# Performance work log

Hardware: AMD Instinct MI355X
Metric: run time of the kernel (lower is better)

## Reference

```python
import jax, jax.numpy as jnp
import numpy as np

NEG_INF = -1.0e12  # matches masked_fill value in the torch module


def _entmax15(x, axis=-1):
    """Exact entmax with alpha=1.5 (Peters & Martins, 2019), sort-based."""
    x = x - jnp.max(x, axis=axis, keepdims=True)
    x = x / 2.0
    d = x.shape[axis]
    xs = -jnp.sort(-x, axis=axis)  # descending sort along normalization axis
    rho = jnp.arange(1, d + 1, dtype=x.dtype)  # 1..d, broadcasts on last axis
    mean = jnp.cumsum(xs, axis=axis) / rho
    mean_sq = jnp.cumsum(xs * xs, axis=axis) / rho
    ss = rho * (mean_sq - mean * mean)
    delta = (1.0 - ss) / rho
    tau = mean - jnp.sqrt(jnp.clip(delta, 0.0))
    support = jnp.sum((tau <= xs).astype(jnp.int32), axis=axis, keepdims=True)
    tau_star = jnp.take_along_axis(tau, support - 1, axis=axis)
    y = jnp.clip(x - tau_star, 0.0)
    return y * y


def setup_inputs() -> dict:
    key = jax.random.key(0)
    kq, kk, kv, km = jax.random.split(key, 4)
    B, H, S, D = 4, 8, 1024, 128
    q = jax.random.normal(kq, (B, H, S, D), dtype=jnp.float32)
    k = jax.random.normal(kk, (B, H, S, D), dtype=jnp.float32)
    v = jax.random.normal(kv, (B, H, S, D), dtype=jnp.float32)
    mask = jax.random.randint(km, (B, 1, S, S), 0, 2, dtype=jnp.int32)
    return {"q": q, "k": k, "v": v, "mask": mask}


def reference(q, k, v, mask):
    D = q.shape[-1]
    scale = 1.0 / jnp.sqrt(jnp.asarray(D, dtype=q.dtype))
    scores = jnp.einsum("bhqd,bhkd->bhqk", q, k) * scale
    scores = jnp.where(mask == 0, jnp.asarray(NEG_INF, dtype=scores.dtype), scores)
    attn = _entmax15(scores, axis=-1)
    return jnp.einsum("bhqk,bhkd->bhqd", attn, v)
```

## Files before the change

### kernel.cpp

```cpp
#include <hip/hip_runtime.h>


#define S_ 1024
#define D_ 128
#define NEG_INF_F (-1.0e12f)
#define SCALE_F 0.08838834764831845f
#define NITER 14

typedef float f32x4 __attribute__((ext_vector_type(4)));
typedef short short8 __attribute__((ext_vector_type(8)));

__device__ __forceinline__ ushort f2bf(float x) {
    unsigned u = __builtin_bit_cast(unsigned, x);
    u += 0x7FFFu + ((u >> 16) & 1u);
    return (ushort)(u >> 16);
}
__device__ __forceinline__ float bf2f(ushort h) {
    unsigned u = ((unsigned)h) << 16;
    return __builtin_bit_cast(float, u);
}

__global__ __launch_bounds__(256)
void pre_cvt(const float* __restrict__ K, const float* __restrict__ V,
             ushort* __restrict__ Kb, ushort* __restrict__ Vt)
{
    __shared__ __align__(16) ushort tileT[64][68];
    const int t = threadIdx.x;
    if (blockIdx.x < 4096) {
        int i = blockIdx.x * 256 + t;
        float4 v = ((const float4*)K)[i];
        ushort4 o;
        o.x = f2bf(v.x); o.y = f2bf(v.y); o.z = f2bf(v.z); o.w = f2bf(v.w);
        ((ushort4*)Kb)[i] = o;
        return;
    }
    const int vb = blockIdx.x - 4096;
    const int bh = vb >> 5, r5 = vb & 31, kt = r5 >> 1, dh = r5 & 1;
    const float* src = V + ((size_t)(bh * S_ + kt * 64)) * D_ + dh * 64;
    #pragma unroll
    for (int i = 0; i < 4; ++i) {
        int idx = t + i * 256, r = idx >> 4, c = idx & 15;
        float4 vv = *(const float4*)(src + (size_t)r * D_ + c * 4);
        tileT[c * 4 + 0][r] = f2bf(vv.x);
        tileT[c * 4 + 1][r] = f2bf(vv.y);
        tileT[c * 4 + 2][r] = f2bf(vv.z);
        tileT[c * 4 + 3][r] = f2bf(vv.w);
    }
    __syncthreads();
    ushort* dst = Vt + ((size_t)(bh * D_ + dh * 64)) * S_ + kt * 64;
    #pragma unroll
    for (int i = 0; i < 2; ++i) {
        int idx = t + i * 256, d = idx >> 3, jj = idx & 7;
        short8 val = *(const short8*)&tileT[d][jj * 8];
        *(short8*)(dst + (size_t)d * S_ + jj * 8) = val;
    }
}

__global__ __launch_bounds__(512, 8)
void entmax_attn(const float* __restrict__ Q, const ushort* __restrict__ Kb,
                 const ushort* __restrict__ Vt, const int* __restrict__ M,
                 float* __restrict__ O)
{
    __shared__ __align__(16) ushort sc[16][1024];
    __shared__ __align__(16) ushort q_s[16][128];

    const int t = threadIdx.x;
    const int w = t >> 6, lane = t & 63, l = lane & 15, quad = lane >> 4;
    const int bh = blockIdx.x >> 6, qt = blockIdx.x & 63, b = bh >> 3;

    const ushort* kb_bh = Kb + (size_t)bh * (S_ * D_);
    const ushort* vt_bh = Vt + (size_t)bh * (D_ * S_);

    {
        const float4* qsrc = (const float4*)(Q + ((size_t)bh * S_ + (size_t)qt * 16) * D_);
        int r = t >> 5, c = t & 31;
        float4 v = qsrc[r * 32 + c];
        ushort4 o;
        o.x = f2bf(v.x); o.y = f2bf(v.y); o.z = f2bf(v.z); o.w = f2bf(v.w);
        *(ushort4*)&q_s[r][(((c >> 1) ^ (r & 7)) << 3) + ((c & 1) << 2)] = o;
    }

    const ushort* kp = kb_bh + (size_t)(w * 16 + l) * D_ + quad * 8;
    short8 c0 = *(const short8*)(kp +  0);
    short8 c1 = *(const short8*)(kp + 32);
    short8 c2 = *(const short8*)(kp + 64);
    short8 c3 = *(const short8*)(kp + 96);

    __syncthreads();

    short8 aq[4];
    #pragma unroll
    for (int ks = 0; ks < 4; ++ks)
        aq[ks] = *(const short8*)&q_s[l][((ks * 4 + quad) ^ (l & 7)) << 3];

    #pragma unroll 1
    for (int kt = 0; kt < 7; ++kt) {
        const ushort* np = kp + (size_t)(kt + 1) * (128 * D_);
        short8 n0 = *(const short8*)(np +  0);
        short8 n1 = *(const short8*)(np + 32);
        short8 n2 = *(const short8*)(np + 64);
        short8 n3 = *(const short8*)(np + 96);
        f32x4 acc = {0.f, 0.f, 0.f, 0.f};
        __builtin_amdgcn_s_setprio(1);
        acc = __builtin_amdgcn_mfma_f32_16x16x32_bf16(aq[0], c0, acc, 0, 0, 0);
        acc = __builtin_amdgcn_mfma_f32_16x16x32_bf16(aq[1], c1, acc, 0, 0, 0);
        acc = __builtin_amdgcn_mfma_f32_16x16x32_bf16(aq[2], c2, acc, 0, 0, 0);
        acc = __builtin_amdgcn_mfma_f32_16x16x32_bf16(aq[3], c3, acc, 0, 0, 0);
        __builtin_amdgcn_s_setprio(0);
        const int coln = kt * 16 + w * 2 + (l >> 3);
        #pragma unroll
        for (int r = 0; r < 4; ++r) {
            const int rr = quad * 4 + r;
            sc[rr][((coln ^ (rr & 7)) << 3) + (l & 7)] = f2bf(acc[r] * SCALE_F);
        }
        c0 = n0; c1 = n1; c2 = n2; c3 = n3;
    }
    {
        f32x4 acc = {0.f, 0.f, 0.f, 0.f};
        __builtin_amdgcn_s_setprio(1);
        acc = __builtin_amdgcn_mfma_f32_16x16x32_bf16(aq[0], c0, acc, 0, 0, 0);
        acc = __builtin_amdgcn_mfma_f32_16x16x32_bf16(aq[1], c1, acc, 0, 0, 0);
        acc = __builtin_amdgcn_mfma_f32_16x16x32_bf16(aq[2], c2, acc, 0, 0, 0);
        acc = __builtin_amdgcn_mfma_f32_16x16x32_bf16(aq[3], c3, acc, 0, 0, 0);
        __builtin_amdgcn_s_setprio(0);
        const int coln = 7 * 16 + w * 2 + (l >> 3);
        #pragma unroll
        for (int r = 0; r < 4; ++r) {
            const int rr = quad * 4 + r;
            sc[rr][((coln ^ (rr & 7)) << 3) + (l & 7)] = f2bf(acc[r] * SCALE_F);
        }
    }
    __syncthreads();

    const int row = t >> 5, u = t & 31;
    const int qg = qt * 16 + row;
    float x[32];
    #pragma unroll
    for (int c = 0; c < 4; ++c) {
        short8 v8 = *(const short8*)&sc[row][((c * 32 + u) ^ (row & 7)) << 3];
        #pragma unroll
        for (int e = 0; e < 8; ++e) x[c * 8 + e] = bf2f(((ushort*)&v8)[e]);
    }
    {
        const int4* mrow = (const int4*)(M + ((size_t)b * S_ + qg) * S_);
        #pragma unroll
        for (int c = 0; c < 4; ++c) {
            #pragma unroll
            for (int h = 0; h < 2; ++h) {
                int4 mm = mrow[c * 64 + u * 2 + h];
                if (mm.x == 0) x[c * 8 + h * 4 + 0] = NEG_INF_F;
                if (mm.y == 0) x[c * 8 + h * 4 + 1] = NEG_INF_F;
                if (mm.z == 0) x[c * 8 + h * 4 + 2] = NEG_INF_F;
                if (mm.w == 0) x[c * 8 + h * 4 + 3] = NEG_INF_F;
            }
        }
    }
    float mx = -3.0e38f;
    #pragma unroll
    for (int j = 0; j < 32; ++j) mx = fmaxf(mx, x[j]);
    #pragma unroll
    for (int off = 1; off < 32; off <<= 1) mx = fmaxf(mx, __shfl_xor(mx, off));
    #pragma unroll
    for (int j = 0; j < 32; ++j) x[j] = (x[j] - mx) * 0.5f;

    float lo = -1.f, hi = 0.f;
    #pragma unroll 1
    for (int it = 0; it < NITER; ++it) {
        const float tm = 0.5f * (lo + hi);
        float f = 0.f;
        #pragma unroll
        for (int j = 0; j < 32; ++j) {
            float d = fmaxf(x[j] - tm, 0.f);
            f = fmaf(d, d, f);
        }
        #pragma unroll
        for (int off = 1; off < 32; off <<= 1) f += __shfl_xor(f, off);
        const bool ge = (f >= 1.f);
        lo = ge ? tm : lo;
        hi = ge ? hi : tm;
    }
    const float tau = 0.5f * (lo + hi);

    #pragma unroll
    for (int c = 0; c < 4; ++c) {
        short8 v8;
        #pragma unroll
        for (int e = 0; e < 8; ++e) {
            float d = fmaxf(x[c * 8 + e] - tau, 0.f);
            ((ushort*)&v8)[e] = f2bf(d * d);
        }
        *(short8*)&sc[row][((c * 32 + u) ^ (row & 7)) << 3] = v8;
    }

    const ushort* vp = vt_bh + (size_t)(w * 16 + l) * S_ + quad * 8;
    c0 = *(const short8*)(vp +  0);
    c1 = *(const short8*)(vp + 32);
    c2 = *(const short8*)(vp + 64);
    c3 = *(const short8*)(vp + 96);
    __syncthreads();

    f32x4 oa = {0.f, 0.f, 0.f, 0.f};
    #pragma unroll 1
    for (int vt = 0; vt < 7; ++vt) {
        const ushort* np = vp + (size_t)(vt + 1) * 128;
        short8 n0 = *(const short8*)(np +  0);
        short8 n1 = *(const short8*)(np + 32);
        short8 n2 = *(const short8*)(np + 64);
        short8 n3 = *(const short8*)(np + 96);
        short8 a0 = *(const short8*)&sc[l][((vt * 16 +  0 + quad) ^ (l & 7)) << 3];
        short8 a1 = *(const short8*)&sc[l][((vt * 16 +  4 + quad) ^ (l & 7)) << 3];
        short8 a2 = *(const short8*)&sc[l][((vt * 16 +  8 + quad) ^ (l & 7)) << 3];
        short8 a3 = *(const short8*)&sc[l][((vt * 16 + 12 + quad) ^ (l & 7)) << 3];
        __builtin_amdgcn_s_setprio(1);
        oa = __builtin_amdgcn_mfma_f32_16x16x32_bf16(a0, c0, oa, 0, 0, 0);
        oa = __builtin_amdgcn_mfma_f32_16x16x32_bf16(a1, c1, oa, 0, 0, 0);
        oa = __builtin_amdgcn_mfma_f32_16x16x32_bf16(a2, c2, oa, 0, 0, 0);
        oa = __builtin_amdgcn_mfma_f32_16x16x32_bf16(a3, c3, oa, 0, 0, 0);
        __builtin_amdgcn_s_setprio(0);
        c0 = n0; c1 = n1; c2 = n2; c3 = n3;
    }
    {
        short8 a0 = *(const short8*)&sc[l][((7 * 16 +  0 + quad) ^ (l & 7)) << 3];
        short8 a1 = *(const short8*)&sc[l][((7 * 16 +  4 + quad) ^ (l & 7)) << 3];
        short8 a2 = *(const short8*)&sc[l][((7 * 16 +  8 + quad) ^ (l & 7)) << 3];
        short8 a3 = *(const short8*)&sc[l][((7 * 16 + 12 + quad) ^ (l & 7)) << 3];
        __builtin_amdgcn_s_setprio(1);
        oa = __builtin_amdgcn_mfma_f32_16x16x32_bf16(a0, c0, oa, 0, 0, 0);
        oa = __builtin_amdgcn_mfma_f32_16x16x32_bf16(a1, c1, oa, 0, 0, 0);
        oa = __builtin_amdgcn_mfma_f32_16x16x32_bf16(a2, c2, oa, 0, 0, 0);
        oa = __builtin_amdgcn_mfma_f32_16x16x32_bf16(a3, c3, oa, 0, 0, 0);
        __builtin_amdgcn_s_setprio(0);
    }

    float* ob = O + ((size_t)bh * S_ + (size_t)qt * 16) * D_;
    #pragma unroll
    for (int r = 0; r < 4; ++r)
        ob[(size_t)(quad * 4 + r) * D_ + w * 16 + l] = oa[r];
}

extern "C" void kernel_launch(void* const* d_in, const int* in_sizes, int n_in,
                              void* d_out, int out_size, void* d_ws, size_t ws_size,
                              hipStream_t stream) {
    const float* q = (const float*)d_in[0];
    const float* k = (const float*)d_in[1];
    const float* v = (const float*)d_in[2];
    const int*   m = (const int*)d_in[3];
    float*       o = (float*)d_out;

    ushort* Kb = (ushort*)d_ws;
    ushort* Vt = (ushort*)((char*)d_ws + 8388608);

    pre_cvt<<<5120, 256, 0, stream>>>(k, v, Kb, Vt);
    entmax_attn<<<2048, 512, 0, stream>>>(q, Kb, Vt, m, o);
}
```

Baseline: 226.9 us.

## Fuse K bf16 conversion into attention kernel, load Q directly to registers

Drops the separate K-to-bf16 conversion pass and reads fp32 K straight from global memory inside the attention kernel, converting to bf16 in registers before each MFMA. Q is also loaded and converted directly into MFMA operand registers, so the shared-memory Q staging and one barrier are gone. The aim is to cut a full K read/write round trip and shrink the pre-pass. In exchange the main kernel reads twice as many bytes for K per block, with K re-read by all 64 query-tile blocks, and uses more registers, so the launch bound occupancy hint is lowered from 8 to 6.

```diff
diff --git a/kernel.cpp b/kernel.cpp
--- a/kernel.cpp
+++ b/kernel.cpp
@@ -19,22 +19,19 @@
     unsigned u = ((unsigned)h) << 16;
     return __builtin_bit_cast(float, u);
 }
+__device__ __forceinline__ short8 cvt8(float4 a, float4 b) {
+    short8 r; ushort* p = (ushort*)&r;
+    p[0] = f2bf(a.x); p[1] = f2bf(a.y); p[2] = f2bf(a.z); p[3] = f2bf(a.w);
+    p[4] = f2bf(b.x); p[5] = f2bf(b.y); p[6] = f2bf(b.z); p[7] = f2bf(b.w);
+    return r;
+}
 
 __global__ __launch_bounds__(256)
-void pre_cvt(const float* __restrict__ K, const float* __restrict__ V,
-             ushort* __restrict__ Kb, ushort* __restrict__ Vt)
+void pre_vt(const float* __restrict__ V, ushort* __restrict__ Vt)
 {
     __shared__ __align__(16) ushort tileT[64][68];
     const int t = threadIdx.x;
-    if (blockIdx.x < 4096) {
-        int i = blockIdx.x * 256 + t;
-        float4 v = ((const float4*)K)[i];
-        ushort4 o;
-        o.x = f2bf(v.x); o.y = f2bf(v.y); o.z = f2bf(v.z); o.w = f2bf(v.w);
-        ((ushort4*)Kb)[i] = o;
-        return;
-    }
-    const int vb = blockIdx.x - 4096;
+    const int vb = blockIdx.x;
     const int bh = vb >> 5, r5 = vb & 31, kt = r5 >> 1, dh = r5 & 1;
     const float* src = V + ((size_t)(bh * S_ + kt * 64)) * D_ + dh * 64;
     #pragma unroll
@@ -56,74 +53,58 @@
     }
 }
 
-__global__ __launch_bounds__(512, 8)
-void entmax_attn(const float* __restrict__ Q, const ushort* __restrict__ Kb,
+__global__ __launch_bounds__(512, 6)
+void entmax_attn(const float* __restrict__ Q, const float* __restrict__ K,
                  const ushort* __restrict__ Vt, const int* __restrict__ M,
                  float* __restrict__ O)
 {
     __shared__ __align__(16) ushort sc[16][1024];
-    __shared__ __align__(16) ushort q_s[16][128];
 
     const int t = threadIdx.x;
     const int w = t >> 6, lane = t & 63, l = lane & 15, quad = lane >> 4;
     const int bh = blockIdx.x >> 6, qt = blockIdx.x & 63, b = bh >> 3;
 
-    const ushort* kb_bh = Kb + (size_t)bh * (S_ * D_);
-    const ushort* vt_bh = Vt + (size_t)bh * (D_ * S_);
-
+    short8 aq[4];
     {
-        const float4* qsrc = (const float4*)(Q + ((size_t)bh * S_ + (size_t)qt * 16) * D_);
-        int r = t >> 5, c = t & 31;
-        float4 v = qsrc[r * 32 + c];
-        ushort4 o;
-        o.x = f2bf(v.x); o.y = f2bf(v.y); o.z = f2bf(v.z); o.w = f2bf(v.w);
-        *(ushort4*)&q_s[r][(((c >> 1) ^ (r & 7)) << 3) + ((c & 1) << 2)] = o;
-    }
-
-    const ushort* kp = kb_bh + (size_t)(w * 16 + l) * D_ + quad * 8;
-    short8 c0 = *(const short8*)(kp +  0);
-    short8 c1 = *(const short8*)(kp + 32);
-    short8 c2 = *(const short8*)(kp + 64);
-    short8 c3 = *(const short8*)(kp + 96);
-
-    __syncthreads();
-
-    short8 aq[4];
-    #pragma unroll
-    for (int ks = 0; ks < 4; ++ks)
-        aq[ks] = *(const short8*)&q_s[l][((ks * 4 + quad) ^ (l & 7)) << 3];
+        const float* qr = Q + ((size_t)(bh * S_ + qt * 16 + l)) * D_ + quad * 8;
+        #pragma unroll
+        for (int ks = 0; ks < 4; ++ks) {
+            float4 qa = *(const float4*)(qr + ks * 32);
+            float4 qb = *(const float4*)(qr + ks * 32 + 4);
+            aq[ks] = cvt8(qa, qb);
+        }
+    }
+
+    const float* kp = K + ((size_t)(bh * S_ + w * 16 + l)) * D_ + quad * 8;
+
+    float4 fA0 = *(const float4*)(kp +  0), fA1 = *(const float4*)(kp +  4);
+    float4 fA2 = *(const float4*)(kp + 32), fA3 = *(const float4*)(kp + 36);
+    float4 fB0 = *(const float4*)(kp + 64), fB1 = *(const float4*)(kp + 68);
+    float4 fB2 = *(const float4*)(kp + 96), fB3 = *(const float4*)(kp + 100);
 
     #pragma unroll 1
-    for (int kt = 0; kt < 7; ++kt) {
-        const ushort* np = kp + (size_t)(kt + 1) * (128 * D_);
-        short8 n0 = *(const short8*)(np +  0);
-        short8 n1 = *(const short8*)(np + 32);
-        short8 n2 = *(const short8*)(np + 64);
-        short8 n3 = *(const short8*)(np + 96);
+    for (int kt = 0; kt < 8; ++kt) {
+        const float* np = kp + (size_t)(kt + 1) * (128 * D_);
         f32x4 acc = {0.f, 0.f, 0.f, 0.f};
-        __builtin_amdgcn_s_setprio(1);
-        acc = __builtin_amdgcn_mfma_f32_16x16x32_bf16(aq[0], c0, acc, 0, 0, 0);
-        acc = __builtin_amdgcn_mfma_f32_16x16x32_bf16(aq[1], c1, acc, 0, 0, 0);
-        acc = __builtin_amdgcn_mfma_f32_16x16x32_bf16(aq[2], c2, acc, 0, 0, 0);
-        acc = __builtin_amdgcn_mfma_f32_16x16x32_bf16(aq[3], c3, acc, 0, 0, 0);
+        short8 b0 = cvt8(fA0, fA1), b1 = cvt8(fA2, fA3);
+        if (kt < 7) {
+            fA0 = *(const float4*)(np +  0); fA1 = *(const float4*)(np +  4);
+            fA2 = *(const float4*)(np + 32); fA3 = *(const float4*)(np + 36);
+        }
+        __builtin_amdgcn_s_setprio(1);
+        acc = __builtin_amdgcn_mfma_f32_16x16x32_bf16(aq[0], b0, acc, 0, 0, 0);
+        acc = __builtin_amdgcn_mfma_f32_16x16x32_bf16(aq[1], b1, acc, 0, 0, 0);
+        __builtin_amdgcn_s_setprio(0);
+        short8 b2 = cvt8(fB0, fB1), b3 = cvt8(fB2, fB3);
+        if (kt < 7) {
+            fB0 = *(const float4*)(np + 64); fB1 = *(const float4*)(np + 68);
+            fB2 = *(const float4*)(np + 96); fB3 = *(const float4*)(np + 100);
+        }
+        __builtin_amdgcn_s_setprio(1);
+        acc = __builtin_amdgcn_mfma_f32_16x16x32_bf16(aq[2], b2, acc, 0, 0, 0);
+        acc = __builtin_amdgcn_mfma_f32_16x16x32_bf16(aq[3], b3, acc, 0, 0, 0);
         __builtin_amdgcn_s_setprio(0);
         const int coln = kt * 16 + w * 2 + (l >> 3);
-        #pragma unroll
-        for (int r = 0; r < 4; ++r) {
-            const int rr = quad * 4 + r;
-            sc[rr][((coln ^ (rr & 7)) << 3) + (l & 7)] = f2bf(acc[r] * SCALE_F);
-        }
-        c0 = n0; c1 = n1; c2 = n2; c3 = n3;
-    }
-    {
-        f32x4 acc = {0.f, 0.f, 0.f, 0.f};
-        __builtin_amdgcn_s_setprio(1);
-        acc = __builtin_amdgcn_mfma_f32_16x16x32_bf16(aq[0], c0, acc, 0, 0, 0);
-        acc = __builtin_amdgcn_mfma_f32_16x16x32_bf16(aq[1], c1, acc, 0, 0, 0);
-        acc = __builtin_amdgcn_mfma_f32_16x16x32_bf16(aq[2], c2, acc, 0, 0, 0);
-        acc = __builtin_amdgcn_mfma_f32_16x16x32_bf16(aq[3], c3, acc, 0, 0, 0);
-        __builtin_amdgcn_s_setprio(0);
-        const int coln = 7 * 16 + w * 2 + (l >> 3);
         #pragma unroll
         for (int r = 0; r < 4; ++r) {
             const int rr = quad * 4 + r;
@@ -192,11 +173,11 @@
         *(short8*)&sc[row][((c * 32 + u) ^ (row & 7)) << 3] = v8;
     }
 
-    const ushort* vp = vt_bh + (size_t)(w * 16 + l) * S_ + quad * 8;
-    c0 = *(const short8*)(vp +  0);
-    c1 = *(const short8*)(vp + 32);
-    c2 = *(const short8*)(vp + 64);
-    c3 = *(const short8*)(vp + 96);
+    const ushort* vp = Vt + (size_t)bh * (D_ * S_) + (size_t)(w * 16 + l) * S_ + quad * 8;
+    short8 c0 = *(const short8*)(vp +  0);
+    short8 c1 = *(const short8*)(vp + 32);
+    short8 c2 = *(const short8*)(vp + 64);
+    short8 c3 = *(const short8*)(vp + 96);
     __syncthreads();
 
     f32x4 oa = {0.f, 0.f, 0.f, 0.f};
@@ -247,9 +228,8 @@
     const int*   m = (const int*)d_in[3];
     float*       o = (float*)d_out;
 
-    ushort* Kb = (ushort*)d_ws;
-    ushort* Vt = (ushort*)((char*)d_ws + 8388608);
-
-    pre_cvt<<<5120, 256, 0, stream>>>(k, v, Kb, Vt);
-    entmax_attn<<<2048, 512, 0, stream>>>(q, Kb, Vt, m, o);
-}
+    ushort* Vt = (ushort*)d_ws;
+
+    pre_vt<<<1024, 256, 0, stream>>>(v, Vt);
+    entmax_attn<<<2048, 512, 0, stream>>>(q, k, Vt, m, o);
+}
```

Result: slower. 303.3 us (+33.7%).
